# Kernel tuning notes

Hardware: AMD Instinct MI355X
Metric: run time of the kernel (lower is better)

Reference implementation:

```python
import jax, jax.numpy as jnp
import numpy as np

N_NODES = 50000
N_EDGES = 800000
HIDDEN = 64
OUT = 16
N_LAYERS = 3


def setup_inputs() -> dict:
    key = jax.random.key(0)
    ks = jax.random.split(key, 8)
    s = 1.0 / np.sqrt(HIDDEN)
    x = jax.random.normal(ks[0], (N_NODES, HIDDEN), dtype=jnp.float32)
    edge_index = jax.random.randint(ks[1], (2, N_EDGES), 0, N_NODES, dtype=jnp.int64)
    # SAGEConv params per layer: lin_l (neighbor path, with bias), lin_r (root path, no bias)
    Wl = jax.random.uniform(ks[2], (N_LAYERS, HIDDEN, HIDDEN), jnp.float32, -s, s)
    bl = jax.random.uniform(ks[3], (N_LAYERS, HIDDEN), jnp.float32, -s, s)
    Wr = jax.random.uniform(ks[4], (N_LAYERS, HIDDEN, HIDDEN), jnp.float32, -s, s)
    W_out = jax.random.uniform(ks[5], (HIDDEN, OUT), jnp.float32, -s, s)
    b_out = jax.random.uniform(ks[6], (OUT,), jnp.float32, -s, s)
    return {"x": x, "edge_index": edge_index, "Wl": Wl, "bl": bl, "Wr": Wr,
            "W_out": W_out, "b_out": b_out}


def reference(x, edge_index, Wl, bl, Wr, W_out, b_out):
    n = x.shape[0]
    src, dst = edge_index[0], edge_index[1]
    # in-degree for mean aggregation (clamped to 1 to avoid div-by-zero)
    deg = jax.ops.segment_sum(jnp.ones((src.shape[0],), x.dtype), dst, num_segments=n)
    deg = jnp.maximum(deg, 1.0)[:, None]  # [N, 1]
    for l in range(N_LAYERS):
        msg = x[src]                                            # [E, H] gather
        agg = jax.ops.segment_sum(msg, dst, num_segments=n) / deg  # scatter-mean [N, H]
        # SAGEConv: lin_l(agg) + lin_r(x)  (lin_r has no bias)
        x = agg @ Wl[l] + bl[l] + x @ Wr[l]
        x = jax.nn.relu(x)
    return x @ W_out + b_out
```

## Files before the change

### kernel.cpp

```cpp
#include <hip/hip_runtime.h>
#include <hip/hip_bf16.h>

#define NN 50000
#define NE 800000
#define HD 64
#define OD 16
#define CAP 64
#define TILES 3125
#define AST 72
#define SCATB 2048
#define PSZ 6250

typedef unsigned short u16;
typedef unsigned int u32;
typedef __attribute__((ext_vector_type(8))) short short8;
typedef __attribute__((ext_vector_type(4))) float f32x4;

__device__ __forceinline__ float bf2f(u16 v) { return __uint_as_float(((u32)v) << 16); }
__device__ __forceinline__ u16 f2bf(float f) {
  __hip_bfloat16 h = __float2bfloat16(f);
  return *reinterpret_cast<u16*>(&h);
}
__device__ __forceinline__ float ldf(const void* p, long i, bool f32m) {
  return f32m ? ((const float*)p)[i] : bf2f(((const u16*)p)[i]);
}
__device__ __forceinline__ int edge_at(const void* eidx, long pos, bool i64) {
  return i64 ? (int)((const long long*)eidx)[pos] : ((const int*)eidx)[pos];
}

__device__ __forceinline__ bool detect_i64(const u32* e32, int lane) {
  return __ballot(e32[2 * lane + 1] != 0u) == 0ull;
}
__device__ __forceinline__ bool detect_f32(const u32* x32, int lane) {
  u32 v = x32[lane] & 0xffffu;
  int e = (int)((v >> 7) & 0xff);
  bool wild = (v != 0u) && (e < 100 || e > 140);
  return __popcll(__ballot(wild)) > 16;
}

__global__ __launch_bounds__(256) void k_pre(
    const void* __restrict__ x, const void* __restrict__ eidx,
    const void* __restrict__ Wl, const void* __restrict__ bl,
    const void* __restrict__ Wr, const void* __restrict__ Wo,
    const void* __restrict__ bo,
    int* __restrict__ deg, u16* __restrict__ csr, u32* __restrict__ spill,
    u16* __restrict__ xA, u16* __restrict__ wfrag, u16* __restrict__ pfrag,
    float* __restrict__ blf, float* __restrict__ bof,
    int* __restrict__ flags) {
  int lane = threadIdx.x & 63;
  if (blockIdx.x < SCATB) {
    bool i64 = detect_i64((const u32*)eidx, lane);
    int g = blockIdx.x & 7;
    int lo = g * PSZ, hi = lo + PSZ;
    int base = (blockIdx.x >> 3) * 256 + threadIdx.x;
    for (int e = base; e < NE; e += 65536) {
      int dst = edge_at(eidx, (long)NE + e, i64);
      if (dst >= lo && dst < hi) {
        int src = edge_at(eidx, e, i64);
        int pos = atomicAdd(&deg[dst], 1);
        if (pos < CAP) csr[(long)dst * CAP + pos] = (u16)src;
        else {
          int sp = atomicAdd(&flags[4], 1);
          spill[sp] = (u32)dst * 50000u + (u32)src;
        }
      }
    }
  } else {
    bool f32m = detect_f32((const u32*)x, lane);
    int i = (blockIdx.x - SCATB) * 256 + threadIdx.x;
    if (f32m) {
      float4 v = ((const float4*)x)[i];
      u32 lo = (u32)f2bf(v.x) | ((u32)f2bf(v.y) << 16);
      u32 hi = (u32)f2bf(v.z) | ((u32)f2bf(v.w) << 16);
      ((u32*)xA)[2 * i] = lo;
      ((u32*)xA)[2 * i + 1] = hi;
    }
    if (i < 3 * 16 * 64 * 8) {
      int j = i & 7, ln = (i >> 3) & 63, f = (i >> 9) & 15, l = i >> 13;
      int s = f >> 2, c = f & 3;
      int k = 32 * s + ((ln >> 4) << 3) + j;
      int n = (c << 4) + (ln & 15);
      long wbase = (long)l * HD * HD;
      float v = (k < HD) ? ldf(Wl, wbase + (long)k * HD + n, f32m)
                         : ldf(Wr, wbase + (long)(k - HD) * HD + n, f32m);
      wfrag[i] = f2bf(v);
    }
    if (i < 2 * 64 * 8) {
      int j = i & 7, ln = (i >> 3) & 63, s = i >> 9;
      int k = 32 * s + ((ln >> 4) << 3) + j;
      pfrag[i] = f2bf(ldf(Wo, (long)k * OD + (ln & 15), f32m));
    }
    if (i < 3 * HD) blf[i] = ldf(bl, i, f32m);
    if (i < OD) bof[i] = ldf(bo, i, f32m);
  }
}

__global__ __launch_bounds__(256, 8) void k_fused(
    const u16* __restrict__ xin_bf, const u16* __restrict__ xin_f32m,
    const u32* __restrict__ xorig32, u16* __restrict__ xout,
    const int* __restrict__ deg, const u16* __restrict__ csr,
    const u32* __restrict__ spill,
    const u16* __restrict__ wfrag, const u16* __restrict__ pfrag,
    const float* __restrict__ bl3, const float* __restrict__ bof,
    void* __restrict__ outp, int layer, int doProj,
    const int* __restrict__ flags) {
  __shared__ __align__(16) u16 aw[16 * AST];
  __shared__ float sbl[HD];
  __shared__ float sbo[OD];
  if (threadIdx.x < HD) sbl[threadIdx.x] = bl3[layer * HD + threadIdx.x];
  if (threadIdx.x < OD) sbo[threadIdx.x] = bof[threadIdx.x];
  int lane = threadIdx.x & 63;
  bool f32m = detect_f32(xorig32, lane);
  int spillcnt = __builtin_amdgcn_readfirstlane(flags[4]);
  const u16* xin = f32m ? xin_f32m : xin_bf;
  const u32* x32 = (const u32*)xin;

  int w = threadIdx.x >> 6;
  int nb = blockIdx.x * 16;
  int fl = lane & 31;
  int half = lane >> 5;
  u32* aw32 = (u32*)aw;
  int n0 = nb + 4 * w;

  int4 dv = *(const int4*)(deg + n0);
  int dt[4] = {__builtin_amdgcn_readfirstlane(dv.x),
               __builtin_amdgcn_readfirstlane(dv.y),
               __builtin_amdgcn_readfirstlane(dv.z),
               __builtin_amdgcn_readfirstlane(dv.w)};
  int idx[4];
#pragma unroll
  for (int g = 0; g < 4; ++g) {
    int d = dt[g] < CAP ? dt[g] : CAP;
    idx[g] = (lane < d) ? (int)csr[(long)(n0 + g) * CAP + lane] : 0;
  }

  for (int g = 0; g < 4; ++g) {
    int dtot = dt[g];
    int d = dtot < CAP ? dtot : CAP;
    float ax0 = 0.f, ay0 = 0.f, ax1 = 0.f, ay1 = 0.f;
    for (int j = 0; j < d; j += 16) {
      u32 v[8];
#pragma unroll
      for (int p = 0; p < 8; ++p) {
        int se = __builtin_amdgcn_readlane(idx[g], j + 2 * p);
        int so = __builtin_amdgcn_readlane(idx[g], j + 2 * p + 1);
        int s = half ? so : se;
        v[p] = x32[(long)s * 32 + fl];
      }
#pragma unroll
      for (int p = 0; p < 8; ++p) {
        int m = j + 2 * p + half;
        u32 vv = (m < d) ? v[p] : 0u;
        float vlo = __uint_as_float(vv << 16);
        float vhi = __uint_as_float(vv & 0xffff0000u);
        if (p & 1) { ax1 += vlo; ay1 += vhi; }
        else       { ax0 += vlo; ay0 += vhi; }
      }
    }
    float ax = ax0 + ax1, ay = ay0 + ay1;
    ax += __shfl_xor(ax, 32);
    ay += __shfl_xor(ay, 32);
    if (spillcnt > 0) {
      int n = n0 + g;
      for (int base = 0; base < spillcnt; base += 64) {
        u32 p = (base + lane < spillcnt) ? spill[base + lane] : 0xffffffffu;
        u32 dd = p / 50000u;
        u32 ss = p - dd * 50000u;
        unsigned long long mk = __ballot(dd == (u32)n);
        while (mk) {
          int j = __builtin_ctzll(mk);
          mk &= mk - 1;
          int s = __builtin_amdgcn_readlane((int)ss, j);
          u32 v = x32[(long)s * 32 + fl];
          ax += __uint_as_float(v << 16);
          ay += __uint_as_float(v & 0xffff0000u);
        }
      }
    }
    float rd = 1.0f / (float)(dtot > 0 ? dtot : 1);
    if (half == 0)
      aw32[(4 * w + g) * (AST / 2) + fl] =
          (u32)f2bf(ax * rd) | ((u32)f2bf(ay * rd) << 16);
  }
  __syncthreads();

  int quad = lane >> 4, m16 = lane & 15;
  short8 a0 = *(const short8*)(aw + m16 * AST + quad * 8);
  short8 a1 = *(const short8*)(aw + m16 * AST + 32 + quad * 8);
  const u16* xrow = xin + (long)(nb + m16) * HD;
  short8 x2 = *(const short8*)(xrow + quad * 8);
  short8 x3 = *(const short8*)(xrow + 32 + quad * 8);
  int c = w;
  const short8* bp = (const short8*)(wfrag + (long)layer * 16 * 64 * 8);
  short8 b0 = bp[(0 * 4 + c) * 64 + lane];
  short8 b1 = bp[(1 * 4 + c) * 64 + lane];
  short8 b2 = bp[(2 * 4 + c) * 64 + lane];
  short8 b3 = bp[(3 * 4 + c) * 64 + lane];
  float bb = sbl[c * 16 + m16];
  f32x4 acc = (f32x4){bb, bb, bb, bb};
  acc = __builtin_amdgcn_mfma_f32_16x16x32_bf16(a0, b0, acc, 0, 0, 0);
  acc = __builtin_amdgcn_mfma_f32_16x16x32_bf16(a1, b1, acc, 0, 0, 0);
  acc = __builtin_amdgcn_mfma_f32_16x16x32_bf16(x2, b2, acc, 0, 0, 0);
  acc = __builtin_amdgcn_mfma_f32_16x16x32_bf16(x3, b3, acc, 0, 0, 0);
  __syncthreads();

#pragma unroll
  for (int r = 0; r < 4; ++r)
    aw[(quad * 4 + r) * AST + c * 16 + m16] = f2bf(fmaxf(acc[r], 0.f));
  __syncthreads();

  if (!doProj) {
    int row = threadIdx.x >> 4, ch = threadIdx.x & 15;
    uint2 v = *(const uint2*)(aw + row * AST + ch * 4);
    *(uint2*)(xout + (long)(nb + row) * HD + ch * 4) = v;
  } else if (w == 0) {
    short8 pa0 = *(const short8*)(aw + m16 * AST + quad * 8);
    short8 pa1 = *(const short8*)(aw + m16 * AST + 32 + quad * 8);
    const short8* pb = (const short8*)pfrag;
    short8 pb0 = pb[lane];
    short8 pb1 = pb[64 + lane];
    float bv = sbo[m16];
    f32x4 pacc = (f32x4){bv, bv, bv, bv};
    pacc = __builtin_amdgcn_mfma_f32_16x16x32_bf16(pa0, pb0, pacc, 0, 0, 0);
    pacc = __builtin_amdgcn_mfma_f32_16x16x32_bf16(pa1, pb1, pacc, 0, 0, 0);
    if (f32m) {
      float* o = (float*)outp;
#pragma unroll
      for (int r = 0; r < 4; ++r)
        o[(long)(nb + quad * 4 + r) * OD + m16] = pacc[r];
    } else {
      u16* o = (u16*)outp;
#pragma unroll
      for (int r = 0; r < 4; ++r)
        o[(long)(nb + quad * 4 + r) * OD + m16] = f2bf(pacc[r]);
    }
  }
}

extern "C" void kernel_launch(void* const* d_in, const int* in_sizes, int n_in,
                              void* d_out, int out_size, void* d_ws, size_t ws_size,
                              hipStream_t stream) {
  const void* x = d_in[0];
  const void* eidx = d_in[1];
  const void* Wl = d_in[2];
  const void* bl = d_in[3];
  const void* Wr = d_in[4];
  const void* Wo = d_in[5];
  const void* bo = d_in[6];

  char* w = (char*)d_ws;
  size_t off = 0;
  int* flags = (int*)(w + off);     off += 256;
  int* deg = (int*)(w + off);       off += (size_t)NN * 4 + 192;
  size_t memset_bytes = off;
  u16* csr = (u16*)(w + off);       off += (size_t)NN * CAP * 2;
  u32* spill = (u32*)(w + off);     off += (size_t)NE * 4;
  u16* wfrag = (u16*)(w + off);     off += 3 * 16 * 64 * 8 * 2;
  u16* pfrag = (u16*)(w + off);     off += 2 * 64 * 8 * 2;
  float* blf = (float*)(w + off);   off += 3 * HD * 4;
  float* bof = (float*)(w + off);   off += 256;
  u16* xA = (u16*)(w + off);        off += (size_t)NN * HD * 2;
  u16* xB = (u16*)(w + off);        off += (size_t)NN * HD * 2;

  hipMemsetAsync(flags, 0, memset_bytes, stream);

  k_pre<<<SCATB + 3125, 256, 0, stream>>>(x, eidx, Wl, bl, Wr, Wo, bo,
                                          deg, csr, spill, xA, wfrag, pfrag,
                                          blf, bof, flags);

  const u32* xo32 = (const u32*)x;
  k_fused<<<TILES, 256, 0, stream>>>((const u16*)x, xA, xo32, xB, deg, csr, spill,
                                     wfrag, pfrag, blf, bof, (void*)0, 0, 0, flags);
  k_fused<<<TILES, 256, 0, stream>>>(xB, xB, xo32, xA, deg, csr, spill,
                                     wfrag, pfrag, blf, bof, (void*)0, 1, 0, flags);
  k_fused<<<TILES, 256, 0, stream>>>(xA, xA, xo32, (u16*)0, deg, csr, spill,
                                     wfrag, pfrag, blf, bof, d_out, 2, 1, flags);
}
```

Baseline: 190.6 us.

## Merge three layer launches into one cooperative persistent kernel with grid sync

Replaces the three per-layer kernel launches with a single cooperative launch of a persistent grid (2048 blocks) that loops over node tiles and synchronises the whole grid between layers. If the cooperative launch fails, it falls back to three ordinary launches of the same kernel. The aim is to remove launch gaps and per-kernel tail effects. In exchange it adds grid-barrier cost, limits the grid to resident blocks, and makes each block run tiles sequentially with more __syncthreads calls.

```diff
diff --git a/kernel.cpp b/kernel.cpp
--- a/kernel.cpp
+++ b/kernel.cpp
@@ -1,5 +1,8 @@
 #include <hip/hip_runtime.h>
 #include <hip/hip_bf16.h>
+#include <hip/hip_cooperative_groups.h>
+
+namespace cg = cooperative_groups;
 
 #define NN 50000
 #define NE 800000
@@ -10,6 +13,7 @@
 #define AST 72
 #define SCATB 2048
 #define PSZ 6250
+#define LGRID 2048
 
 typedef unsigned short u16;
 typedef unsigned int u32;
@@ -95,145 +99,155 @@
   }
 }
 
-__global__ __launch_bounds__(256, 8) void k_fused(
-    const u16* __restrict__ xin_bf, const u16* __restrict__ xin_f32m,
-    const u32* __restrict__ xorig32, u16* __restrict__ xout,
+__global__ __launch_bounds__(256, 8) void k_layers(
+    const u16* __restrict__ xbf, u16* __restrict__ xA, u16* __restrict__ xB,
+    const u32* __restrict__ xorig32,
     const int* __restrict__ deg, const u16* __restrict__ csr,
     const u32* __restrict__ spill,
     const u16* __restrict__ wfrag, const u16* __restrict__ pfrag,
     const float* __restrict__ bl3, const float* __restrict__ bof,
-    void* __restrict__ outp, int layer, int doProj,
-    const int* __restrict__ flags) {
+    void* __restrict__ outp, const int* __restrict__ flags,
+    int l0, int l1) {
   __shared__ __align__(16) u16 aw[16 * AST];
   __shared__ float sbl[HD];
   __shared__ float sbo[OD];
-  if (threadIdx.x < HD) sbl[threadIdx.x] = bl3[layer * HD + threadIdx.x];
-  if (threadIdx.x < OD) sbo[threadIdx.x] = bof[threadIdx.x];
   int lane = threadIdx.x & 63;
   bool f32m = detect_f32(xorig32, lane);
   int spillcnt = __builtin_amdgcn_readfirstlane(flags[4]);
-  const u16* xin = f32m ? xin_f32m : xin_bf;
-  const u32* x32 = (const u32*)xin;
-
   int w = threadIdx.x >> 6;
-  int nb = blockIdx.x * 16;
   int fl = lane & 31;
   int half = lane >> 5;
   u32* aw32 = (u32*)aw;
-  int n0 = nb + 4 * w;
-
-  int4 dv = *(const int4*)(deg + n0);
-  int dt[4] = {__builtin_amdgcn_readfirstlane(dv.x),
-               __builtin_amdgcn_readfirstlane(dv.y),
-               __builtin_amdgcn_readfirstlane(dv.z),
-               __builtin_amdgcn_readfirstlane(dv.w)};
-  int idx[4];
-#pragma unroll
-  for (int g = 0; g < 4; ++g) {
-    int d = dt[g] < CAP ? dt[g] : CAP;
-    idx[g] = (lane < d) ? (int)csr[(long)(n0 + g) * CAP + lane] : 0;
-  }
-
-  for (int g = 0; g < 4; ++g) {
-    int dtot = dt[g];
-    int d = dtot < CAP ? dtot : CAP;
-    float ax0 = 0.f, ay0 = 0.f, ax1 = 0.f, ay1 = 0.f;
-    for (int j = 0; j < d; j += 16) {
-      u32 v[8];
-#pragma unroll
-      for (int p = 0; p < 8; ++p) {
-        int se = __builtin_amdgcn_readlane(idx[g], j + 2 * p);
-        int so = __builtin_amdgcn_readlane(idx[g], j + 2 * p + 1);
-        int s = half ? so : se;
-        v[p] = x32[(long)s * 32 + fl];
+  int quad = lane >> 4, m16 = lane & 15;
+  if (threadIdx.x < OD) sbo[threadIdx.x] = bof[threadIdx.x];
+
+  for (int layer = l0; layer < l1; ++layer) {
+    const u16* xin = (layer == 0) ? (f32m ? xA : xbf)
+                                  : ((layer == 1) ? (const u16*)xB : (const u16*)xA);
+    u16* xout = (layer == 0) ? xB : ((layer == 1) ? xA : (u16*)0);
+    int doProj = (layer == 2);
+    const u32* x32 = (const u32*)xin;
+    if (threadIdx.x < HD) sbl[threadIdx.x] = bl3[layer * HD + threadIdx.x];
+
+    for (int tile = blockIdx.x; tile < TILES; tile += LGRID) {
+      int nb = tile * 16;
+      int n0 = nb + 4 * w;
+
+      int4 dv = *(const int4*)(deg + n0);
+      int dt[4] = {__builtin_amdgcn_readfirstlane(dv.x),
+                   __builtin_amdgcn_readfirstlane(dv.y),
+                   __builtin_amdgcn_readfirstlane(dv.z),
+                   __builtin_amdgcn_readfirstlane(dv.w)};
+      int idx[4];
+#pragma unroll
+      for (int g = 0; g < 4; ++g) {
+        int d = dt[g] < CAP ? dt[g] : CAP;
+        idx[g] = (lane < d) ? (int)csr[(long)(n0 + g) * CAP + lane] : 0;
       }
-#pragma unroll
-      for (int p = 0; p < 8; ++p) {
-        int m = j + 2 * p + half;
-        u32 vv = (m < d) ? v[p] : 0u;
-        float vlo = __uint_as_float(vv << 16);
-        float vhi = __uint_as_float(vv & 0xffff0000u);
-        if (p & 1) { ax1 += vlo; ay1 += vhi; }
-        else       { ax0 += vlo; ay0 += vhi; }
+
+      for (int g = 0; g < 4; ++g) {
+        int dtot = dt[g];
+        int d = dtot < CAP ? dtot : CAP;
+        float ax0 = 0.f, ay0 = 0.f, ax1 = 0.f, ay1 = 0.f;
+        for (int j = 0; j < d; j += 16) {
+          u32 v[8];
+#pragma unroll
+          for (int p = 0; p < 8; ++p) {
+            int se = __builtin_amdgcn_readlane(idx[g], j + 2 * p);
+            int so = __builtin_amdgcn_readlane(idx[g], j + 2 * p + 1);
+            int s = half ? so : se;
+            v[p] = x32[(long)s * 32 + fl];
+          }
+#pragma unroll
+          for (int p = 0; p < 8; ++p) {
+            int m = j + 2 * p + half;
+            u32 vv = (m < d) ? v[p] : 0u;
+            float vlo = __uint_as_float(vv << 16);
+            float vhi = __uint_as_float(vv & 0xffff0000u);
+            if (p & 1) { ax1 += vlo; ay1 += vhi; }
+            else       { ax0 += vlo; ay0 += vhi; }
+          }
+        }
+        float ax = ax0 + ax1, ay = ay0 + ay1;
+        ax += __shfl_xor(ax, 32);
+        ay += __shfl_xor(ay, 32);
+        if (spillcnt > 0) {
+          int n = n0 + g;
+          for (int base = 0; base < spillcnt; base += 64) {
+            u32 p = (base + lane < spillcnt) ? spill[base + lane] : 0xffffffffu;
+            u32 dd = p / 50000u;
+            u32 ss = p - dd * 50000u;
+            unsigned long long mk = __ballot(dd == (u32)n);
+            while (mk) {
+              int j = __builtin_ctzll(mk);
+              mk &= mk - 1;
+              int s = __builtin_amdgcn_readlane((int)ss, j);
+              u32 v = x32[(long)s * 32 + fl];
+              ax += __uint_as_float(v << 16);
+              ay += __uint_as_float(v & 0xffff0000u);
+            }
+          }
+        }
+        float rd = 1.0f / (float)(dtot > 0 ? dtot : 1);
+        if (half == 0)
+          aw32[(4 * w + g) * (AST / 2) + fl] =
+              (u32)f2bf(ax * rd) | ((u32)f2bf(ay * rd) << 16);
       }
-    }
-    float ax = ax0 + ax1, ay = ay0 + ay1;
-    ax += __shfl_xor(ax, 32);
-    ay += __shfl_xor(ay, 32);
-    if (spillcnt > 0) {
-      int n = n0 + g;
-      for (int base = 0; base < spillcnt; base += 64) {
-        u32 p = (base + lane < spillcnt) ? spill[base + lane] : 0xffffffffu;
-        u32 dd = p / 50000u;
-        u32 ss = p - dd * 50000u;
-        unsigned long long mk = __ballot(dd == (u32)n);
-        while (mk) {
-          int j = __builtin_ctzll(mk);
-          mk &= mk - 1;
-          int s = __builtin_amdgcn_readlane((int)ss, j);
-          u32 v = x32[(long)s * 32 + fl];
-          ax += __uint_as_float(v << 16);
-          ay += __uint_as_float(v & 0xffff0000u);
+      __syncthreads();
+
+      short8 a0 = *(const short8*)(aw + m16 * AST + quad * 8);
+      short8 a1 = *(const short8*)(aw + m16 * AST + 32 + quad * 8);
+      const u16* xrow = xin + (long)(nb + m16) * HD;
+      short8 x2 = *(const short8*)(xrow + quad * 8);
+      short8 x3 = *(const short8*)(xrow + 32 + quad * 8);
+      int c = w;
+      const short8* bp = (const short8*)(wfrag + (long)layer * 16 * 64 * 8);
+      short8 b0 = bp[(0 * 4 + c) * 64 + lane];
+      short8 b1 = bp[(1 * 4 + c) * 64 + lane];
+      short8 b2 = bp[(2 * 4 + c) * 64 + lane];
+      short8 b3 = bp[(3 * 4 + c) * 64 + lane];
+      float bb = sbl[c * 16 + m16];
+      f32x4 acc = (f32x4){bb, bb, bb, bb};
+      acc = __builtin_amdgcn_mfma_f32_16x16x32_bf16(a0, b0, acc, 0, 0, 0);
+      acc = __builtin_amdgcn_mfma_f32_16x16x32_bf16(a1, b1, acc, 0, 0, 0);
+      acc = __builtin_amdgcn_mfma_f32_16x16x32_bf16(x2, b2, acc, 0, 0, 0);
+      acc = __builtin_amdgcn_mfma_f32_16x16x32_bf16(x3, b3, acc, 0, 0, 0);
+      __syncthreads();
+
+#pragma unroll
+      for (int r = 0; r < 4; ++r)
+        aw[(quad * 4 + r) * AST + c * 16 + m16] = f2bf(fmaxf(acc[r], 0.f));
+      __syncthreads();
+
+      if (!doProj) {
+        int row = threadIdx.x >> 4, ch = threadIdx.x & 15;
+        uint2 vv = *(const uint2*)(aw + row * AST + ch * 4);
+        *(uint2*)(xout + (long)(nb + row) * HD + ch * 4) = vv;
+      } else if (w == 0) {
+        short8 pa0 = *(const short8*)(aw + m16 * AST + quad * 8);
+        short8 pa1 = *(const short8*)(aw + m16 * AST + 32 + quad * 8);
+        const short8* pb = (const short8*)pfrag;
+        short8 pb0 = pb[lane];
+        short8 pb1 = pb[64 + lane];
+        float bv = sbo[m16];
+        f32x4 pacc = (f32x4){bv, bv, bv, bv};
+        pacc = __builtin_amdgcn_mfma_f32_16x16x32_bf16(pa0, pb0, pacc, 0, 0, 0);
+        pacc = __builtin_amdgcn_mfma_f32_16x16x32_bf16(pa1, pb1, pacc, 0, 0, 0);
+        if (f32m) {
+          float* o = (float*)outp;
+#pragma unroll
+          for (int r = 0; r < 4; ++r)
+            o[(long)(nb + quad * 4 + r) * OD + m16] = pacc[r];
+        } else {
+          u16* o = (u16*)outp;
+#pragma unroll
+          for (int r = 0; r < 4; ++r)
+            o[(long)(nb + quad * 4 + r) * OD + m16] = f2bf(pacc[r]);
         }
       }
-    }
-    float rd = 1.0f / (float)(dtot > 0 ? dtot : 1);
-    if (half == 0)
-      aw32[(4 * w + g) * (AST / 2) + fl] =
-          (u32)f2bf(ax * rd) | ((u32)f2bf(ay * rd) << 16);
-  }
-  __syncthreads();
-
-  int quad = lane >> 4, m16 = lane & 15;
-  short8 a0 = *(const short8*)(aw + m16 * AST + quad * 8);
-  short8 a1 = *(const short8*)(aw + m16 * AST + 32 + quad * 8);
-  const u16* xrow = xin + (long)(nb + m16) * HD;
-  short8 x2 = *(const short8*)(xrow + quad * 8);
-  short8 x3 = *(const short8*)(xrow + 32 + quad * 8);
-  int c = w;
-  const short8* bp = (const short8*)(wfrag + (long)layer * 16 * 64 * 8);
-  short8 b0 = bp[(0 * 4 + c) * 64 + lane];
-  short8 b1 = bp[(1 * 4 + c) * 64 + lane];
-  short8 b2 = bp[(2 * 4 + c) * 64 + lane];
-  short8 b3 = bp[(3 * 4 + c) * 64 + lane];
-  float bb = sbl[c * 16 + m16];
-  f32x4 acc = (f32x4){bb, bb, bb, bb};
-  acc = __builtin_amdgcn_mfma_f32_16x16x32_bf16(a0, b0, acc, 0, 0, 0);
-  acc = __builtin_amdgcn_mfma_f32_16x16x32_bf16(a1, b1, acc, 0, 0, 0);
-  acc = __builtin_amdgcn_mfma_f32_16x16x32_bf16(x2, b2, acc, 0, 0, 0);
-  acc = __builtin_amdgcn_mfma_f32_16x16x32_bf16(x3, b3, acc, 0, 0, 0);
-  __syncthreads();
-
-#pragma unroll
-  for (int r = 0; r < 4; ++r)
-    aw[(quad * 4 + r) * AST + c * 16 + m16] = f2bf(fmaxf(acc[r], 0.f));
-  __syncthreads();
-
-  if (!doProj) {
-    int row = threadIdx.x >> 4, ch = threadIdx.x & 15;
-    uint2 v = *(const uint2*)(aw + row * AST + ch * 4);
-    *(uint2*)(xout + (long)(nb + row) * HD + ch * 4) = v;
-  } else if (w == 0) {
-    short8 pa0 = *(const short8*)(aw + m16 * AST + quad * 8);
-    short8 pa1 = *(const short8*)(aw + m16 * AST + 32 + quad * 8);
-    const short8* pb = (const short8*)pfrag;
-    short8 pb0 = pb[lane];
-    short8 pb1 = pb[64 + lane];
-    float bv = sbo[m16];
-    f32x4 pacc = (f32x4){bv, bv, bv, bv};
-    pacc = __builtin_amdgcn_mfma_f32_16x16x32_bf16(pa0, pb0, pacc, 0, 0, 0);
-    pacc = __builtin_amdgcn_mfma_f32_16x16x32_bf16(pa1, pb1, pacc, 0, 0, 0);
-    if (f32m) {
-      float* o = (float*)outp;
-#pragma unroll
-      for (int r = 0; r < 4; ++r)
-        o[(long)(nb + quad * 4 + r) * OD + m16] = pacc[r];
-    } else {
-      u16* o = (u16*)outp;
-#pragma unroll
-      for (int r = 0; r < 4; ++r)
-        o[(long)(nb + quad * 4 + r) * OD + m16] = f2bf(pacc[r]);
-    }
+      __syncthreads();
+    }
+    if (layer + 1 < l1) cg::this_grid().sync();
   }
 }
 
@@ -268,11 +282,20 @@
                                           deg, csr, spill, xA, wfrag, pfrag,
                                           blf, bof, flags);
 
+  const u16* xbf = (const u16*)x;
   const u32* xo32 = (const u32*)x;
-  k_fused<<<TILES, 256, 0, stream>>>((const u16*)x, xA, xo32, xB, deg, csr, spill,
-                                     wfrag, pfrag, blf, bof, (void*)0, 0, 0, flags);
-  k_fused<<<TILES, 256, 0, stream>>>(xB, xB, xo32, xA, deg, csr, spill,
-                                     wfrag, pfrag, blf, bof, (void*)0, 1, 0, flags);
-  k_fused<<<TILES, 256, 0, stream>>>(xA, xA, xo32, (u16*)0, deg, csr, spill,
-                                     wfrag, pfrag, blf, bof, d_out, 2, 1, flags);
-}
+  void* outp = d_out;
+  int l0 = 0, l1 = 3;
+  void* kargs[] = {(void*)&xbf, (void*)&xA, (void*)&xB, (void*)&xo32,
+                   (void*)&deg, (void*)&csr, (void*)&spill, (void*)&wfrag,
+                   (void*)&pfrag, (void*)&blf, (void*)&bof, (void*)&outp,
+                   (void*)&flags, (void*)&l0, (void*)&l1};
+  hipError_t ce = hipLaunchCooperativeKernel((void*)k_layers, dim3(LGRID),
+                                             dim3(256), kargs, 0, stream);
+  if (ce != hipSuccess) {
+    for (int l = 0; l < 3; ++l)
+      k_layers<<<LGRID, 256, 0, stream>>>(xbf, xA, xB, xo32, deg, csr, spill,
+                                          wfrag, pfrag, blf, bof, outp, flags,
+                                          l, l + 1);
+  }
+}
```

Result: slower. 723.9 us (+279.8%).

## Software-pipeline neighbor gathers with 8-byte loads and 4 edges per instruction

Applied to the files above, without the earlier changes.

Reworks the mean-aggregation gather so each wavefront handles 4 edges per load with 16 lanes each fetching 8 bytes (uint2), instead of 2 edges with 32 lanes of 4 bytes. The CSR indices for all 4 nodes are fetched in a single vector load and unpacked from u16 pairs. The gathers for the next node are issued before the current node is reduced, using double buffers, so memory latency overlaps with accumulation. This costs more registers and an extra shuffle-reduce stage, and it adds a clamp on indices.

```diff
diff --git a/kernel.cpp b/kernel.cpp
--- a/kernel.cpp
+++ b/kernel.cpp
@@ -113,12 +113,12 @@
   bool f32m = detect_f32(xorig32, lane);
   int spillcnt = __builtin_amdgcn_readfirstlane(flags[4]);
   const u16* xin = f32m ? xin_f32m : xin_bf;
-  const u32* x32 = (const u32*)xin;
+  const uint2* x2p = (const uint2*)xin;
 
   int w = threadIdx.x >> 6;
   int nb = blockIdx.x * 16;
-  int fl = lane & 31;
-  int half = lane >> 5;
+  int q = lane >> 4;
+  int f = lane & 15;
   u32* aw32 = (u32*)aw;
   int n0 = nb + 4 * w;
 
@@ -127,61 +127,98 @@
                __builtin_amdgcn_readfirstlane(dv.y),
                __builtin_amdgcn_readfirstlane(dv.z),
                __builtin_amdgcn_readfirstlane(dv.w)};
-  int idx[4];
-#pragma unroll
-  for (int g = 0; g < 4; ++g) {
-    int d = dt[g] < CAP ? dt[g] : CAP;
-    idx[g] = (lane < d) ? (int)csr[(long)(n0 + g) * CAP + lane] : 0;
+  uint2 cidx = ((const uint2*)(csr + (long)n0 * CAP))[lane];
+
+#define LOADB(dst, gg, jj)                                                    \
+  do {                                                                        \
+    _Pragma("unroll") for (int p = 0; p < 8; ++p) {                           \
+      u32 wx = (u32)__builtin_amdgcn_readlane((int)cidx.x,                    \
+                                              (gg)*16 + ((jj) >> 2) + p);     \
+      u32 wy = (u32)__builtin_amdgcn_readlane((int)cidx.y,                    \
+                                              (gg)*16 + ((jj) >> 2) + p);     \
+      u32 ww = (q & 2) ? wy : wx;                                             \
+      int s = (int)((ww >> ((q & 1) * 16)) & 0xffffu);                        \
+      s = s < NN ? s : 0;     \
+      dst[p] = x2p[(long)s * 16 + f];                                         \
+    }                                                                         \
+  } while (0)
+
+#define CONSB(vv, gg)                                                         \
+  do {                                                                        \
+    int dtot = dt[gg];                                                        \
+    int d = dtot < CAP ? dtot : CAP;                                          \
+    float a0 = 0.f, a1 = 0.f, a2 = 0.f, a3 = 0.f;                             \
+    _Pragma("unroll") for (int p = 0; p < 8; ++p) {                           \
+      bool val = (4 * p + q) < d;                                             \
+      u32 lo = val ? (u32)vv[p].x : 0u;                                       \
+      u32 hi = val ? (u32)vv[p].y : 0u;                                       \
+      a0 += __uint_as_float(lo << 16);                                        \
+      a1 += __uint_as_float(lo & 0xffff0000u);                                \
+      a2 += __uint_as_float(hi << 16);                                        \
+      a3 += __uint_as_float(hi & 0xffff0000u);                                \
+    }                                                                         \
+    if (d > 32) {                        \
+      _Pragma("unroll") for (int p = 0; p < 8; ++p) {                         \
+        u32 wx = (u32)__builtin_amdgcn_readlane((int)cidx.x, (gg)*16 + 8 + p);\
+        u32 wy = (u32)__builtin_amdgcn_readlane((int)cidx.y, (gg)*16 + 8 + p);\
+        u32 ww = (q & 2) ? wy : wx;                                           \
+        int s = (int)((ww >> ((q & 1) * 16)) & 0xffffu);                      \
+        s = s < NN ? s : 0;                                                   \
+        uint2 t = x2p[(long)s * 16 + f];                                      \
+        bool val = (32 + 4 * p + q) < d;                                      \
+        u32 lo = val ? (u32)t.x : 0u;                                         \
+        u32 hi = val ? (u32)t.y : 0u;                                         \
+        a0 += __uint_as_float(lo << 16);                                      \
+        a1 += __uint_as_float(lo & 0xffff0000u);                              \
+        a2 += __uint_as_float(hi << 16);                                      \
+        a3 += __uint_as_float(hi & 0xffff0000u);                              \
+      }                                                                       \
+    }                                                                         \
+    a0 += __shfl_xor(a0, 16); a1 += __shfl_xor(a1, 16);                       \
+    a2 += __shfl_xor(a2, 16); a3 += __shfl_xor(a3, 16);                       \
+    a0 += __shfl_xor(a0, 32); a1 += __shfl_xor(a1, 32);                       \
+    a2 += __shfl_xor(a2, 32); a3 += __shfl_xor(a3, 32);                       \
+    if (spillcnt > 0) {        \
+      int n = n0 + (gg);                                                      \
+      for (int base = 0; base < spillcnt; base += 64) {                       \
+        u32 pp = (base + lane < spillcnt) ? spill[base + lane] : 0xffffffffu; \
+        u32 dd = pp / 50000u;                                                 \
+        u32 ss = pp - dd * 50000u;                                            \
+        unsigned long long mk = __ballot(dd == (u32)n);                       \
+        while (mk) {                                                          \
+          int j = __builtin_ctzll(mk);                                        \
+          mk &= mk - 1;                                                       \
+          int s = __builtin_amdgcn_readlane((int)ss, j);                      \
+          uint2 t = x2p[(long)s * 16 + f];                                    \
+          a0 += __uint_as_float(((u32)t.x) << 16);                            \
+          a1 += __uint_as_float(((u32)t.x) & 0xffff0000u);                    \
+          a2 += __uint_as_float(((u32)t.y) << 16);                            \
+          a3 += __uint_as_float(((u32)t.y) & 0xffff0000u);                    \
+        }                                                                     \
+      }                                                                       \
+    }                                                                         \
+    float rd = 1.0f / (float)(dtot > 0 ? dtot : 1);                           \
+    if (q == 0) {                        \
+      u32 plo = (u32)f2bf(a0 * rd) | ((u32)f2bf(a1 * rd) << 16);              \
+      u32 phi = (u32)f2bf(a2 * rd) | ((u32)f2bf(a3 * rd) << 16);              \
+      *(uint2*)(aw32 + (4 * w + (gg)) * (AST / 2) + 2 * f) =                  \
+          make_uint2(plo, phi);                                               \
+    }                                                                         \
+  } while (0)
+
+  {
+    uint2 va[8], vb[8];
+    LOADB(va, 0, 0);
+    LOADB(vb, 1, 0);
+    CONSB(va, 0);
+    LOADB(va, 2, 0);
+    CONSB(vb, 1);
+    LOADB(vb, 3, 0);
+    CONSB(va, 2);
+    CONSB(vb, 3);
   }
-
-  for (int g = 0; g < 4; ++g) {
-    int dtot = dt[g];
-    int d = dtot < CAP ? dtot : CAP;
-    float ax0 = 0.f, ay0 = 0.f, ax1 = 0.f, ay1 = 0.f;
-    for (int j = 0; j < d; j += 16) {
-      u32 v[8];
-#pragma unroll
-      for (int p = 0; p < 8; ++p) {
-        int se = __builtin_amdgcn_readlane(idx[g], j + 2 * p);
-        int so = __builtin_amdgcn_readlane(idx[g], j + 2 * p + 1);
-        int s = half ? so : se;
-        v[p] = x32[(long)s * 32 + fl];
-      }
-#pragma unroll
-      for (int p = 0; p < 8; ++p) {
-        int m = j + 2 * p + half;
-        u32 vv = (m < d) ? v[p] : 0u;
-        float vlo = __uint_as_float(vv << 16);
-        float vhi = __uint_as_float(vv & 0xffff0000u);
-        if (p & 1) { ax1 += vlo; ay1 += vhi; }
-        else       { ax0 += vlo; ay0 += vhi; }
-      }
-    }
-    float ax = ax0 + ax1, ay = ay0 + ay1;
-    ax += __shfl_xor(ax, 32);
-    ay += __shfl_xor(ay, 32);
-    if (spillcnt > 0) {
-      int n = n0 + g;
-      for (int base = 0; base < spillcnt; base += 64) {
-        u32 p = (base + lane < spillcnt) ? spill[base + lane] : 0xffffffffu;
-        u32 dd = p / 50000u;
-        u32 ss = p - dd * 50000u;
-        unsigned long long mk = __ballot(dd == (u32)n);
-        while (mk) {
-          int j = __builtin_ctzll(mk);
-          mk &= mk - 1;
-          int s = __builtin_amdgcn_readlane((int)ss, j);
-          u32 v = x32[(long)s * 32 + fl];
-          ax += __uint_as_float(v << 16);
-          ay += __uint_as_float(v & 0xffff0000u);
-        }
-      }
-    }
-    float rd = 1.0f / (float)(dtot > 0 ? dtot : 1);
-    if (half == 0)
-      aw32[(4 * w + g) * (AST / 2) + fl] =
-          (u32)f2bf(ax * rd) | ((u32)f2bf(ay * rd) << 16);
-  }
+#undef LOADB
+#undef CONSB
   __syncthreads();
 
   int quad = lane >> 4, m16 = lane & 15;
```

New measurement: 175.7 us. 1.08x faster.
